# Optimization experiments

Measured on AMD Instinct MI355X. Metric: run time of the kernel, lower is better.

The kernel has to match this reference:

```python
import jax, jax.numpy as jnp
import numpy as np

# HeteNet distribute_compute reference: per-agent expert id (hete_pick) selects one of
# E heterogeneous expert MLPs; tokens are gathered per expert, run through that expert's
# actor net, and scattered back into a padded [n_threads, n_agents, n_action] output.
# Here each expert is a 2-layer MLP (Net._act actor head approximation):
#   logits = relu(x @ W1[e] + b1[e]) @ W2[e] + b2[e]
# The dispatch/combine is expressed as dense per-expert compute + one-hot combine,
# which is the mathematically identical (mask-select) form of the gather/scatter.

T, N, D, H, A, E = 64, 64, 512, 512, 32, 15  # threads, agents, obs_dim(+addon), hidden, actions, experts


def setup_inputs() -> dict:
    key = jax.random.key(0)
    k0, k1, k2, k3 = jax.random.split(key, 4)
    obs = jax.random.normal(k0, (T, N, D), dtype=jnp.float32)
    hete_pick = jax.random.randint(k1, (T, N), 0, E)  # expert id per agent
    W1 = jax.random.normal(k2, (E, D, H), dtype=jnp.float32) * (1.0 / np.sqrt(D))
    b1 = jnp.zeros((E, H), dtype=jnp.float32)
    W2 = jax.random.normal(k3, (E, H, A), dtype=jnp.float32) * (1.0 / np.sqrt(H))
    b2 = jnp.zeros((E, A), dtype=jnp.float32)
    return {"obs": obs, "W1": W1, "b1": b1, "W2": W2, "b2": b2, "hete_pick": hete_pick}


def reference(obs, W1, b1, W2, b2, hete_pick):
    # per-expert dense forward: [E, T, N, H]
    h = jax.nn.relu(jnp.einsum('tnd,edh->etnh', obs, W1) + b1[:, None, None, :])
    logits = jnp.einsum('etnh,eha->etna', h, W2) + b2[:, None, None, :]  # [E,T,N,A]
    # combine: scatter each expert's rows back per mask (hete_pick == e)
    onehot = (hete_pick[None, :, :] == jnp.arange(E)[:, None, None]).astype(obs.dtype)  # [E,T,N]
    return jnp.einsum('etna,etn->tna', logits, onehot)  # [T,N,A]
```

## Files before the change

### kernel.cpp

```cpp
#include <hip/hip_runtime.h>
#include <stdint.h>

#define NTOK 4096
#define DDIM 512
#define HDIM 512
#define ADIM 32
#define NEXP 15
#define TILE_M 32
#define GRID_M 288

typedef __attribute__((ext_vector_type(8))) short bf16x8;
typedef __attribute__((ext_vector_type(8))) unsigned short ushort8;
typedef __attribute__((ext_vector_type(4))) unsigned short ushort4v;
typedef __attribute__((ext_vector_type(4))) float f32x4;

__device__ __forceinline__ unsigned short f2bf(float f) {
  unsigned int u = __float_as_uint(f);
  u += 0x7fffu + ((u >> 16) & 1u);
  return (unsigned short)(u >> 16);
}

__device__ __forceinline__ void gld_lds16(const void* g, void* l) {
  __builtin_amdgcn_global_load_lds(
      (const __attribute__((address_space(1))) void*)g,
      (__attribute__((address_space(3))) void*)l, 16, 0, 0);
}

__global__ __launch_bounds__(256) void prep_kernel(
    const float* __restrict__ W1, const float* __restrict__ W2,
    const int* __restrict__ pick, int* __restrict__ meta,
    int* __restrict__ lists, unsigned short* __restrict__ W1I,
    unsigned short* __restrict__ W2T, float* __restrict__ out)
{
  extern __shared__ char smem[];
  const int bid = blockIdx.x;
  const int tid = threadIdx.x;
  const int x = bid & 7, s = bid >> 3;
  int role, e = 0, kc = 0;
  if (x < 7)       { role = 0; e = 2 * x + (s >> 4); kc = s & 15; }
  else if (s < 16) { role = 0; e = 14; kc = s; }
  else if (s < 31) { role = 1; e = s - 16; }
  else             { role = 2; }

  if (role == 0) {
    float* sm = (float*)smem;
    const int r0 = kc * 32;
    const float* src = W1 + (size_t)e * (DDIM * HDIM) + (size_t)r0 * HDIM;
    #pragma unroll
    for (int v = 0; v < 16; ++v) {
      int i = v * 256 + tid;
      int row = i >> 7, col = (i & 127) * 4;
      *(float4*)(sm + row * 517 + col) = *(const float4*)(src + (size_t)row * 512 + col);
    }
    __syncthreads();
    unsigned short* dst = W1I + (size_t)(e * 16 + kc) * 512 * 32;
    const int p = tid & 3;
    #pragma unroll
    for (int w = 0; w < 8; ++w) {
      int n = w * 64 + (tid >> 2);
      int q = p ^ ((n >> 1) & 3);
      ushort8 vv;
      #pragma unroll
      for (int xx = 0; xx < 8; ++xx) vv[xx] = f2bf(sm[(q * 8 + xx) * 517 + n]);
      *(ushort8*)(dst + (size_t)n * 32 + p * 8) = vv;
    }
  } else if (role == 1) {
    float4 z4; z4.x = 0.f; z4.y = 0.f; z4.z = 0.f; z4.w = 0.f;
    for (int i = e * 256 + tid; i < NTOK * ADIM / 4; i += 15 * 256)
      ((float4*)out)[i] = z4;
    float* sm = (float*)smem;
    const float* src = W2 + (size_t)e * (HDIM * ADIM);
    #pragma unroll
    for (int v = 0; v < 16; ++v) {
      int i = v * 256 + tid;
      int row = i >> 3, col = (i & 7) * 4;
      *(float4*)(sm + row * 36 + col) = *(const float4*)(src + (size_t)row * 32 + col);
    }
    __syncthreads();
    unsigned short* dst = W2T + (size_t)e * (ADIM * HDIM);
    const int a = tid >> 3, k0 = (tid & 7) * 64;
    #pragma unroll
    for (int w = 0; w < 8; ++w) {
      ushort8 vv;
      #pragma unroll
      for (int xx = 0; xx < 8; ++xx) vv[xx] = f2bf(sm[(size_t)(k0 + w * 8 + xx) * 36 + a]);
      *(ushort8*)(dst + (size_t)a * 512 + k0 + w * 8) = vv;
    }
  } else {
    int* s_pos = (int*)smem;
    int* s_wt  = s_pos + NEXP * 256;
    int* s_nt  = s_wt + 64;
    int* s_bse = s_nt + 16;
    const int lane = tid & 63, wv = tid >> 6;
    int pk[16];
    #pragma unroll
    for (int i = 0; i < 16; ++i) pk[i] = pick[tid * 16 + i];
    int c[NEXP], inc[NEXP];
    #pragma unroll
    for (int ee = 0; ee < NEXP; ++ee) {
      int cc = 0;
      #pragma unroll
      for (int i = 0; i < 16; ++i) cc += (pk[i] == ee) ? 1 : 0;
      c[ee] = cc; inc[ee] = cc;
    }
    #pragma unroll
    for (int off = 1; off < 64; off <<= 1) {
      #pragma unroll
      for (int ee = 0; ee < NEXP; ++ee) {
        int v = __shfl_up(inc[ee], off, 64);
        if (lane >= off) inc[ee] += v;
      }
    }
    if (lane == 63) {
      #pragma unroll
      for (int ee = 0; ee < NEXP; ++ee) s_wt[wv * 16 + ee] = inc[ee];
    }
    __syncthreads();
    #pragma unroll
    for (int ee = 0; ee < NEXP; ++ee) {
      int base0 = 0;
      #pragma unroll
      for (int w = 0; w < 4; ++w) if (w < wv) base0 += s_wt[w * 16 + ee];
      s_pos[ee * 256 + tid] = base0 + inc[ee] - c[ee];
    }
    #pragma unroll
    for (int i = 0; i < 16; ++i) {
      int pp = pk[i];
      int pos = s_pos[pp * 256 + tid]++;
      lists[pp * NTOK + pos] = tid * 16 + i;
    }
    if (tid < NEXP) {
      int tot = s_wt[tid] + s_wt[16 + tid] + s_wt[32 + tid] + s_wt[48 + tid];
      meta[tid] = tot;
      s_nt[tid] = (tot + TILE_M - 1) / TILE_M;
    }
    __syncthreads();
    if (tid == 0) {
      int b = 0;
      for (int ee = 0; ee < NEXP; ++ee) { s_bse[ee] = b; b += s_nt[ee]; }
      meta[15] = b;
    }
    __syncthreads();
    if (tid < NEXP) {
      int b = s_bse[tid], nt2 = s_nt[tid];
      for (int i = 0; i < nt2; ++i) meta[16 + b + i] = (tid << 16) | i;
    }
  }
}

__global__ __launch_bounds__(256, 2) void moe_gemm(
    const float* __restrict__ obs, const float* __restrict__ b1,
    const float* __restrict__ b2, const int* __restrict__ meta,
    const int* __restrict__ lists, const unsigned short* __restrict__ W1I,
    const unsigned short* __restrict__ W2T, float* __restrict__ out)
{
  const int ntiles = meta[15];
  const int nphys = ntiles * 2;
  const int p = blockIdx.x;
  const int xq = nphys >> 3, xr = nphys & 7;
  const int xcd = p & 7, slot = p >> 3;
  const int cx = xq + (xcd < xr ? 1 : 0);
  if (slot >= cx) return;
  const int j2 = xcd * xq + (xcd < xr ? xcd : xr) + slot;
  const int jt = j2 >> 1, half = j2 & 1;

  const int tl = meta[16 + jt];
  const int e = tl >> 16;
  const int tile_lo = (tl & 0xffff) * TILE_M;
  const int cnt = meta[e];
  int mvalid = cnt - tile_lo; if (mvalid > TILE_M) mvalid = TILE_M;

  extern __shared__ char smem[];
  char* s_x = smem;
  char* wb0 = smem + 32768;
  char* wb1 = smem + 49152;
  char* wb2 = smem + 65536;

  const int tid = threadIdx.x, lane = tid & 63, wave = tid >> 6;
  const int l15 = lane & 15, l4 = lane >> 4;
  const int nbl = wave * 64;
  const int hbase = half * 256;
  const int* mylist = lists + e * NTOK;
  const unsigned short* w1i_e = W1I + (size_t)e * 16 * 512 * 32;
  const unsigned short* w2t_e = W2T + (size_t)e * (ADIM * HDIM);

  const int m = tid >> 3, s8 = tid & 7;
  int idx = tile_lo + m; if (idx >= cnt) idx = cnt - 1;
  const float* grow = obs + (size_t)mylist[idx] * DDIM;
  float4 xf[16];
  #pragma unroll
  for (int si = 0; si < 8; ++si) {
    xf[si * 2]     = *(const float4*)(grow + (s8 + si * 8) * 8);
    xf[si * 2 + 1] = *(const float4*)(grow + (s8 + si * 8) * 8 + 4);
  }
  __builtin_amdgcn_sched_barrier(0);

  float4 bvv[4];
  #pragma unroll
  for (int nt = 0; nt < 4; ++nt)
    bvv[nt] = *(const float4*)(b1 + e * HDIM + hbase + nbl + nt * 16 + l4 * 4);
  __builtin_amdgcn_sched_barrier(0);

  auto issue_w1 = [&](int t, char* buf) {
    const unsigned short* wbase = w1i_e + (size_t)t * (512 * 32) + (size_t)hbase * 32;
    #pragma unroll
    for (int i = 0; i < 4; ++i) {
      int nb = nbl + i * 16;
      gld_lds16(wbase + (size_t)nb * 32 + lane * 8, buf + nb * 64);
    }
  };
  issue_w1(0, wb0);
  __builtin_amdgcn_sched_barrier(0);
  issue_w1(1, wb1);
  __builtin_amdgcn_sched_barrier(0);

  #pragma unroll
  for (int si = 0; si < 8; ++si) {
    int s = s8 + si * 8;
    float4 f0 = xf[si * 2], f1 = xf[si * 2 + 1];
    ushort8 v;
    v[0] = f2bf(f0.x); v[1] = f2bf(f0.y); v[2] = f2bf(f0.z); v[3] = f2bf(f0.w);
    v[4] = f2bf(f1.x); v[5] = f2bf(f1.y); v[6] = f2bf(f1.z); v[7] = f2bf(f1.w);
    *(ushort8*)(s_x + m * 1024 + ((s ^ (m & 7)) << 4)) = v;
  }
  __syncthreads();

  f32x4 acc[4][2];
  #pragma unroll
  for (int nt = 0; nt < 4; ++nt) {
    f32x4 b4 = {bvv[nt].x, bvv[nt].y, bvv[nt].z, bvv[nt].w};
    acc[nt][0] = b4; acc[nt][1] = b4;
  }

  #pragma unroll
  for (int t = 0; t < 16; ++t) {
    if (t < 14) {
      char* nxt = ((t + 2) % 3 == 0) ? wb0 : ((t + 2) % 3 == 1) ? wb1 : wb2;
      issue_w1(t + 2, nxt);
    } else if (t == 14) {
      #pragma unroll
      for (int i = 0; i < 4; ++i) {
        int o = wave * 4096 + i * 1024 + lane * 16;
        int a = o >> 9;
        int p16 = (o >> 4) & 31;
        gld_lds16(w2t_e + (size_t)a * 512 + hbase + (size_t)((p16 ^ (a & 7)) * 8),
                  wb1 + o);
      }
    }
    if (t < 15) asm volatile("s_waitcnt vmcnt(8)" ::: "memory");
    else        asm volatile("s_waitcnt vmcnt(4)" ::: "memory");
    __builtin_amdgcn_sched_barrier(0);

    const char* cw = (t % 3 == 0) ? wb0 : (t % 3 == 1) ? wb1 : wb2;
    bf16x8 wfr[4], xfr[2];
    #pragma unroll
    for (int nt = 0; nt < 4; ++nt) {
      int n = nbl + nt * 16 + l15;
      wfr[nt] = *(const bf16x8*)(cw + n * 64 + ((l4 ^ ((n >> 1) & 3)) << 4));
    }
    #pragma unroll
    for (int mt = 0; mt < 2; ++mt) {
      int mm = mt * 16 + l15;
      xfr[mt] = *(const bf16x8*)(s_x + mm * 1024 + ((((t << 2) + l4) ^ (mm & 7)) << 4));
    }
    #pragma unroll
    for (int nt = 0; nt < 4; ++nt)
      #pragma unroll
      for (int mt = 0; mt < 2; ++mt)
        acc[nt][mt] = __builtin_amdgcn_mfma_f32_16x16x32_bf16(wfr[nt], xfr[mt], acc[nt][mt], 0, 0, 0);
  }

  __syncthreads();

  #pragma unroll
  for (int nt = 0; nt < 4; ++nt) {
    int n0 = nbl + nt * 16 + l4 * 4;
    int sg = n0 >> 3, hsel = (n0 >> 2) & 1;
    #pragma unroll
    for (int mt = 0; mt < 2; ++mt) {
      int mm = mt * 16 + l15;
      ushort4v hv;
      #pragma unroll
      for (int r = 0; r < 4; ++r) hv[r] = f2bf(fmaxf(acc[nt][mt][r], 0.f));
      *(ushort4v*)(s_x + mm * 1024 + ((sg ^ (mm & 7)) << 4) + hsel * 8) = hv;
    }
  }
  __syncthreads();

  const int mt2 = wave >> 1, at2 = wave & 1;
  const int a2 = at2 * 16 + l15;
  float b2v = half ? 0.f : b2[e * ADIM + a2];
  f32x4 acc2 = {b2v, b2v, b2v, b2v};
  #pragma unroll
  for (int ks = 0; ks < 8; ++ks) {
    int mm = mt2 * 16 + l15;
    bf16x8 af = *(const bf16x8*)(s_x + mm * 1024 + ((((ks << 2) + l4) ^ (mm & 7)) << 4));
    bf16x8 bf = *(const bf16x8*)(wb1 + a2 * 512 + ((((ks << 2) + l4) ^ (a2 & 7)) << 4));
    acc2 = __builtin_amdgcn_mfma_f32_16x16x32_bf16(af, bf, acc2, 0, 0, 0);
  }
  #pragma unroll
  for (int r = 0; r < 4; ++r) {
    int mrow = mt2 * 16 + l4 * 4 + r;
    if (mrow < mvalid)
      atomicAdd(&out[(size_t)mylist[tile_lo + mrow] * ADIM + a2], acc2[r]);
  }
}

__global__ __launch_bounds__(256) void naive_kernel(
    const float* __restrict__ obs, const float* __restrict__ W1,
    const float* __restrict__ b1, const float* __restrict__ W2,
    const float* __restrict__ b2, const int* __restrict__ pick,
    float* __restrict__ out)
{
  __shared__ float sx[DDIM];
  __shared__ float sh[HDIM];
  const int t = blockIdx.x, tid = threadIdx.x;
  const int e = pick[t];
  const float* x = obs + (size_t)t * DDIM;
  for (int i = tid; i < DDIM; i += 256) sx[i] = x[i];
  __syncthreads();
  const float* w1 = W1 + (size_t)e * DDIM * HDIM;
  for (int j = tid; j < HDIM; j += 256) {
    float a = b1[e * HDIM + j];
    for (int d = 0; d < DDIM; ++d) a = fmaf(sx[d], w1[(size_t)d * HDIM + j], a);
    sh[j] = a > 0.f ? a : 0.f;
  }
  __syncthreads();
  if (tid < ADIM) {
    const float* w2 = W2 + (size_t)e * HDIM * ADIM;
    float a = b2[e * ADIM + tid];
    for (int j = 0; j < HDIM; ++j) a = fmaf(sh[j], w2[(size_t)j * ADIM + tid], a);
    out[(size_t)t * ADIM + tid] = a;
  }
}

extern "C" void kernel_launch(void* const* d_in, const int* in_sizes, int n_in,
                              void* d_out, int out_size, void* d_ws, size_t ws_size,
                              hipStream_t stream)
{
  const float* obs = (const float*)d_in[0];
  const float* W1  = (const float*)d_in[1];
  const float* b1  = (const float*)d_in[2];
  const float* W2  = (const float*)d_in[3];
  const float* b2  = (const float*)d_in[4];
  const int* pick  = (const int*)d_in[5];
  float* out = (float*)d_out;
  (void)in_sizes; (void)n_in; (void)out_size;

  const size_t OFF_LISTS = 1024;
  const size_t OFF_W1I   = 262144;
  const size_t OFF_W2T   = OFF_W1I + (size_t)NEXP * HDIM * DDIM * 2;
  const size_t WS_NEEDED = OFF_W2T + (size_t)NEXP * ADIM * HDIM * 2;

  if (ws_size < WS_NEEDED) {
    naive_kernel<<<dim3(NTOK), dim3(256), 0, stream>>>(obs, W1, b1, W2, b2, pick, out);
    return;
  }

  char* ws = (char*)d_ws;
  int* meta   = (int*)ws;
  int* lists  = (int*)(ws + OFF_LISTS);
  unsigned short* W1I = (unsigned short*)(ws + OFF_W1I);
  unsigned short* W2T = (unsigned short*)(ws + OFF_W2T);

  prep_kernel<<<dim3(256), dim3(256), 73728, stream>>>(
      W1, W2, pick, meta, lists, W1I, W2T, out);
  moe_gemm<<<dim3(GRID_M), dim3(256), 81920, stream>>>(
      obs, b1, b2, meta, lists, W1I, W2T, out);
}
```

Measured before the change: 25.42 us.

## Double token tile to 64 rows with 5-stage weight pipeline

Raises the per-block token tile from 32 to 64 rows, so each W1 slice streamed into LDS is reused across twice as many tokens, and deepens the LDS weight ring from 3 to 5 buffers with 4 tiles in flight. The obs load is now converted in a loop after the weight prefetch is issued, and the second GEMM gives each wave 16 rows across both action tiles. Costs are a larger LDS footprint (144KB), occupancy dropping to one block per CU, fewer blocks, and more padding waste on partially filled expert tiles.

```diff
diff --git a/kernel.cpp b/kernel.cpp
--- a/kernel.cpp
+++ b/kernel.cpp
@@ -6,8 +6,8 @@
 #define HDIM 512
 #define ADIM 32
 #define NEXP 15
-#define TILE_M 32
-#define GRID_M 288
+#define TILE_M 64
+#define GRID_M 160
 
 typedef __attribute__((ext_vector_type(8))) short bf16x8;
 typedef __attribute__((ext_vector_type(8))) unsigned short ushort8;
@@ -148,7 +148,7 @@
   }
 }
 
-__global__ __launch_bounds__(256, 2) void moe_gemm(
+__global__ __launch_bounds__(256, 1) void moe_gemm(
     const float* __restrict__ obs, const float* __restrict__ b1,
     const float* __restrict__ b2, const int* __restrict__ meta,
     const int* __restrict__ lists, const unsigned short* __restrict__ W1I,
@@ -172,9 +172,8 @@
 
   extern __shared__ char smem[];
   char* s_x = smem;
-  char* wb0 = smem + 32768;
-  char* wb1 = smem + 49152;
-  char* wb2 = smem + 65536;
+  char* wb[5] = { smem + 65536, smem + 81920, smem + 98304,
+                  smem + 114688, smem + 131072 };
 
   const int tid = threadIdx.x, lane = tid & 63, wave = tid >> 6;
   const int l15 = lane & 15, l4 = lane >> 4;
@@ -184,23 +183,6 @@
   const unsigned short* w1i_e = W1I + (size_t)e * 16 * 512 * 32;
   const unsigned short* w2t_e = W2T + (size_t)e * (ADIM * HDIM);
 
-  const int m = tid >> 3, s8 = tid & 7;
-  int idx = tile_lo + m; if (idx >= cnt) idx = cnt - 1;
-  const float* grow = obs + (size_t)mylist[idx] * DDIM;
-  float4 xf[16];
-  #pragma unroll
-  for (int si = 0; si < 8; ++si) {
-    xf[si * 2]     = *(const float4*)(grow + (s8 + si * 8) * 8);
-    xf[si * 2 + 1] = *(const float4*)(grow + (s8 + si * 8) * 8 + 4);
-  }
-  __builtin_amdgcn_sched_barrier(0);
-
-  float4 bvv[4];
-  #pragma unroll
-  for (int nt = 0; nt < 4; ++nt)
-    bvv[nt] = *(const float4*)(b1 + e * HDIM + hbase + nbl + nt * 16 + l4 * 4);
-  __builtin_amdgcn_sched_barrier(0);
-
   auto issue_w1 = [&](int t, char* buf) {
     const unsigned short* wbase = w1i_e + (size_t)t * (512 * 32) + (size_t)hbase * 32;
     #pragma unroll
@@ -209,64 +191,82 @@
       gld_lds16(wbase + (size_t)nb * 32 + lane * 8, buf + nb * 64);
     }
   };
-  issue_w1(0, wb0);
-  __builtin_amdgcn_sched_barrier(0);
-  issue_w1(1, wb1);
-  __builtin_amdgcn_sched_barrier(0);
-
-  #pragma unroll
-  for (int si = 0; si < 8; ++si) {
-    int s = s8 + si * 8;
-    float4 f0 = xf[si * 2], f1 = xf[si * 2 + 1];
-    ushort8 v;
-    v[0] = f2bf(f0.x); v[1] = f2bf(f0.y); v[2] = f2bf(f0.z); v[3] = f2bf(f0.w);
-    v[4] = f2bf(f1.x); v[5] = f2bf(f1.y); v[6] = f2bf(f1.z); v[7] = f2bf(f1.w);
-    *(ushort8*)(s_x + m * 1024 + ((s ^ (m & 7)) << 4)) = v;
-  }
-  __syncthreads();
-
-  f32x4 acc[4][2];
+  issue_w1(0, wb[0]);
+  __builtin_amdgcn_sched_barrier(0);
+  issue_w1(1, wb[1]);
+  __builtin_amdgcn_sched_barrier(0);
+  issue_w1(2, wb[2]);
+  __builtin_amdgcn_sched_barrier(0);
+  issue_w1(3, wb[3]);
+  __builtin_amdgcn_sched_barrier(0);
+
+  float4 bvv[4];
+  #pragma unroll
+  for (int nt = 0; nt < 4; ++nt)
+    bvv[nt] = *(const float4*)(b1 + e * HDIM + hbase + nbl + nt * 16 + l4 * 4);
+  __builtin_amdgcn_sched_barrier(0);
+
+  {
+    const int m = tid >> 2, sq = tid & 3;
+    int idx = tile_lo + m; if (idx >= cnt) idx = cnt - 1;
+    const float* grow = obs + (size_t)mylist[idx] * DDIM;
+    #pragma unroll 4
+    for (int si = 0; si < 16; ++si) {
+      const int s = sq + si * 4;
+      float4 f0 = *(const float4*)(grow + s * 8);
+      float4 f1 = *(const float4*)(grow + s * 8 + 4);
+      ushort8 v;
+      v[0] = f2bf(f0.x); v[1] = f2bf(f0.y); v[2] = f2bf(f0.z); v[3] = f2bf(f0.w);
+      v[4] = f2bf(f1.x); v[5] = f2bf(f1.y); v[6] = f2bf(f1.z); v[7] = f2bf(f1.w);
+      *(ushort8*)(s_x + m * 1024 + ((s ^ (m & 7)) << 4)) = v;
+    }
+  }
+  __syncthreads();
+
+  f32x4 acc[4][4];
   #pragma unroll
   for (int nt = 0; nt < 4; ++nt) {
     f32x4 b4 = {bvv[nt].x, bvv[nt].y, bvv[nt].z, bvv[nt].w};
-    acc[nt][0] = b4; acc[nt][1] = b4;
+    #pragma unroll
+    for (int mt = 0; mt < 4; ++mt) acc[nt][mt] = b4;
   }
 
   #pragma unroll
   for (int t = 0; t < 16; ++t) {
-    if (t < 14) {
-      char* nxt = ((t + 2) % 3 == 0) ? wb0 : ((t + 2) % 3 == 1) ? wb1 : wb2;
-      issue_w1(t + 2, nxt);
-    } else if (t == 14) {
+    if (t <= 11) {
+      issue_w1(t + 4, wb[(t + 4) % 5]);
+    } else if (t == 12) {
       #pragma unroll
       for (int i = 0; i < 4; ++i) {
         int o = wave * 4096 + i * 1024 + lane * 16;
         int a = o >> 9;
         int p16 = (o >> 4) & 31;
         gld_lds16(w2t_e + (size_t)a * 512 + hbase + (size_t)((p16 ^ (a & 7)) * 8),
-                  wb1 + o);
+                  wb[1] + o);
       }
     }
-    if (t < 15) asm volatile("s_waitcnt vmcnt(8)" ::: "memory");
-    else        asm volatile("s_waitcnt vmcnt(4)" ::: "memory");
+    if (t <= 12)      asm volatile("s_waitcnt vmcnt(16)" ::: "memory");
+    else if (t == 13) asm volatile("s_waitcnt vmcnt(12)" ::: "memory");
+    else if (t == 14) asm volatile("s_waitcnt vmcnt(8)" ::: "memory");
+    else              asm volatile("s_waitcnt vmcnt(4)" ::: "memory");
     __builtin_amdgcn_sched_barrier(0);
 
-    const char* cw = (t % 3 == 0) ? wb0 : (t % 3 == 1) ? wb1 : wb2;
-    bf16x8 wfr[4], xfr[2];
+    const char* cw = wb[t % 5];
+    bf16x8 wfr[4], xfr[4];
     #pragma unroll
     for (int nt = 0; nt < 4; ++nt) {
       int n = nbl + nt * 16 + l15;
       wfr[nt] = *(const bf16x8*)(cw + n * 64 + ((l4 ^ ((n >> 1) & 3)) << 4));
     }
     #pragma unroll
-    for (int mt = 0; mt < 2; ++mt) {
+    for (int mt = 0; mt < 4; ++mt) {
       int mm = mt * 16 + l15;
       xfr[mt] = *(const bf16x8*)(s_x + mm * 1024 + ((((t << 2) + l4) ^ (mm & 7)) << 4));
     }
     #pragma unroll
     for (int nt = 0; nt < 4; ++nt)
       #pragma unroll
-      for (int mt = 0; mt < 2; ++mt)
+      for (int mt = 0; mt < 4; ++mt)
         acc[nt][mt] = __builtin_amdgcn_mfma_f32_16x16x32_bf16(wfr[nt], xfr[mt], acc[nt][mt], 0, 0, 0);
   }
 
@@ -277,7 +277,7 @@
     int n0 = nbl + nt * 16 + l4 * 4;
     int sg = n0 >> 3, hsel = (n0 >> 2) & 1;
     #pragma unroll
-    for (int mt = 0; mt < 2; ++mt) {
+    for (int mt = 0; mt < 4; ++mt) {
       int mm = mt * 16 + l15;
       ushort4v hv;
       #pragma unroll
@@ -287,23 +287,32 @@
   }
   __syncthreads();
 
-  const int mt2 = wave >> 1, at2 = wave & 1;
-  const int a2 = at2 * 16 + l15;
-  float b2v = half ? 0.f : b2[e * ADIM + a2];
-  f32x4 acc2 = {b2v, b2v, b2v, b2v};
+  const int mm2 = wave * 16 + l15;
+  f32x4 acc2[2];
+  #pragma unroll
+  for (int at = 0; at < 2; ++at) {
+    float b2v = half ? 0.f : b2[e * ADIM + at * 16 + l15];
+    f32x4 b4 = {b2v, b2v, b2v, b2v};
+    acc2[at] = b4;
+  }
   #pragma unroll
   for (int ks = 0; ks < 8; ++ks) {
-    int mm = mt2 * 16 + l15;
-    bf16x8 af = *(const bf16x8*)(s_x + mm * 1024 + ((((ks << 2) + l4) ^ (mm & 7)) << 4));
-    bf16x8 bf = *(const bf16x8*)(wb1 + a2 * 512 + ((((ks << 2) + l4) ^ (a2 & 7)) << 4));
-    acc2 = __builtin_amdgcn_mfma_f32_16x16x32_bf16(af, bf, acc2, 0, 0, 0);
-  }
-  #pragma unroll
-  for (int r = 0; r < 4; ++r) {
-    int mrow = mt2 * 16 + l4 * 4 + r;
-    if (mrow < mvalid)
-      atomicAdd(&out[(size_t)mylist[tile_lo + mrow] * ADIM + a2], acc2[r]);
-  }
+    bf16x8 af = *(const bf16x8*)(s_x + mm2 * 1024 + ((((ks << 2) + l4) ^ (mm2 & 7)) << 4));
+    #pragma unroll
+    for (int at = 0; at < 2; ++at) {
+      int a = at * 16 + l15;
+      bf16x8 bf = *(const bf16x8*)(wb[1] + a * 512 + ((((ks << 2) + l4) ^ (a & 7)) << 4));
+      acc2[at] = __builtin_amdgcn_mfma_f32_16x16x32_bf16(af, bf, acc2[at], 0, 0, 0);
+    }
+  }
+  #pragma unroll
+  for (int at = 0; at < 2; ++at)
+    #pragma unroll
+    for (int r = 0; r < 4; ++r) {
+      int mrow = wave * 16 + l4 * 4 + r;
+      if (mrow < mvalid)
+        atomicAdd(&out[(size_t)mylist[tile_lo + mrow] * ADIM + at * 16 + l15], acc2[at][r]);
+    }
 }
 
 __global__ __launch_bounds__(256) void naive_kernel(
@@ -365,6 +374,6 @@
 
   prep_kernel<<<dim3(256), dim3(256), 73728, stream>>>(
       W1, W2, pick, meta, lists, W1I, W2T, out);
-  moe_gemm<<<dim3(GRID_M), dim3(256), 81920, stream>>>(
+  moe_gemm<<<dim3(GRID_M), dim3(256), 147456, stream>>>(
       obs, b1, b2, meta, lists, W1I, W2T, out);
 }
```

Measured after the change: 26.22 us. 1.03x slower.

## Move token routing from prep kernel into each GEMM block

Applied to the files above, without the earlier changes.

The single prep block that counted per-expert tokens and built global routing lists and tile metadata is removed. Each GEMM block now reads all 4096 expert picks, computes per-expert counts and tile mapping with wave reductions, and builds its own 32-token list in shared memory. This takes the serial routing block off the critical path and drops the global meta/list round trip, but every GEMM block now repeats the pick read and extra barriers before its main work.

```diff
diff --git a/kernel.cpp b/kernel.cpp
--- a/kernel.cpp
+++ b/kernel.cpp
@@ -28,9 +28,8 @@
 
 __global__ __launch_bounds__(256) void prep_kernel(
     const float* __restrict__ W1, const float* __restrict__ W2,
-    const int* __restrict__ pick, int* __restrict__ meta,
-    int* __restrict__ lists, unsigned short* __restrict__ W1I,
-    unsigned short* __restrict__ W2T, float* __restrict__ out)
+    unsigned short* __restrict__ W1I, unsigned short* __restrict__ W2T,
+    float* __restrict__ out)
 {
   extern __shared__ char smem[];
   const int bid = blockIdx.x;
@@ -40,7 +39,7 @@
   if (x < 7)       { role = 0; e = 2 * x + (s >> 4); kc = s & 15; }
   else if (s < 16) { role = 0; e = 14; kc = s; }
   else if (s < 31) { role = 1; e = s - 16; }
-  else             { role = 2; }
+  else             { return; }
 
   if (role == 0) {
     float* sm = (float*)smem;
@@ -64,7 +63,7 @@
       for (int xx = 0; xx < 8; ++xx) vv[xx] = f2bf(sm[(q * 8 + xx) * 517 + n]);
       *(ushort8*)(dst + (size_t)n * 32 + p * 8) = vv;
     }
-  } else if (role == 1) {
+  } else {
     float4 z4; z4.x = 0.f; z4.y = 0.f; z4.z = 0.f; z4.w = 0.f;
     for (int i = e * 256 + tid; i < NTOK * ADIM / 4; i += 15 * 256)
       ((float4*)out)[i] = z4;
@@ -86,75 +85,53 @@
       for (int xx = 0; xx < 8; ++xx) vv[xx] = f2bf(sm[(size_t)(k0 + w * 8 + xx) * 36 + a]);
       *(ushort8*)(dst + (size_t)a * 512 + k0 + w * 8) = vv;
     }
-  } else {
-    int* s_pos = (int*)smem;
-    int* s_wt  = s_pos + NEXP * 256;
-    int* s_nt  = s_wt + 64;
-    int* s_bse = s_nt + 16;
-    const int lane = tid & 63, wv = tid >> 6;
-    int pk[16];
-    #pragma unroll
-    for (int i = 0; i < 16; ++i) pk[i] = pick[tid * 16 + i];
-    int c[NEXP], inc[NEXP];
-    #pragma unroll
-    for (int ee = 0; ee < NEXP; ++ee) {
-      int cc = 0;
-      #pragma unroll
-      for (int i = 0; i < 16; ++i) cc += (pk[i] == ee) ? 1 : 0;
-      c[ee] = cc; inc[ee] = cc;
-    }
-    #pragma unroll
-    for (int off = 1; off < 64; off <<= 1) {
-      #pragma unroll
-      for (int ee = 0; ee < NEXP; ++ee) {
-        int v = __shfl_up(inc[ee], off, 64);
-        if (lane >= off) inc[ee] += v;
-      }
-    }
-    if (lane == 63) {
-      #pragma unroll
-      for (int ee = 0; ee < NEXP; ++ee) s_wt[wv * 16 + ee] = inc[ee];
-    }
-    __syncthreads();
-    #pragma unroll
-    for (int ee = 0; ee < NEXP; ++ee) {
-      int base0 = 0;
-      #pragma unroll
-      for (int w = 0; w < 4; ++w) if (w < wv) base0 += s_wt[w * 16 + ee];
-      s_pos[ee * 256 + tid] = base0 + inc[ee] - c[ee];
-    }
-    #pragma unroll
-    for (int i = 0; i < 16; ++i) {
-      int pp = pk[i];
-      int pos = s_pos[pp * 256 + tid]++;
-      lists[pp * NTOK + pos] = tid * 16 + i;
-    }
-    if (tid < NEXP) {
-      int tot = s_wt[tid] + s_wt[16 + tid] + s_wt[32 + tid] + s_wt[48 + tid];
-      meta[tid] = tot;
-      s_nt[tid] = (tot + TILE_M - 1) / TILE_M;
-    }
-    __syncthreads();
-    if (tid == 0) {
-      int b = 0;
-      for (int ee = 0; ee < NEXP; ++ee) { s_bse[ee] = b; b += s_nt[ee]; }
-      meta[15] = b;
-    }
-    __syncthreads();
-    if (tid < NEXP) {
-      int b = s_bse[tid], nt2 = s_nt[tid];
-      for (int i = 0; i < nt2; ++i) meta[16 + b + i] = (tid << 16) | i;
-    }
   }
 }
 
 __global__ __launch_bounds__(256, 2) void moe_gemm(
     const float* __restrict__ obs, const float* __restrict__ b1,
-    const float* __restrict__ b2, const int* __restrict__ meta,
-    const int* __restrict__ lists, const unsigned short* __restrict__ W1I,
-    const unsigned short* __restrict__ W2T, float* __restrict__ out)
+    const float* __restrict__ b2, const int* __restrict__ pick,
+    const unsigned short* __restrict__ W1I, const unsigned short* __restrict__ W2T,
+    float* __restrict__ out)
 {
-  const int ntiles = meta[15];
+  extern __shared__ char smem[];
+  char* s_x = smem;
+  char* wb0 = smem + 32768;
+  char* wb1 = smem + 49152;
+  char* wb2 = smem + 65536;
+  int* s_wt   = (int*)wb2;
+  int* s_we   = (int*)(wb2 + 256);
+  int* s_list = (int*)(wb2 + 320);
+
+  const int tid = threadIdx.x, lane = tid & 63, wave = tid >> 6;
+  const int l15 = lane & 15, l4 = lane >> 4;
+
+  int pk[16];
+  {
+    const int4* pv = (const int4*)pick + tid * 4;
+    int4 q0 = pv[0], q1 = pv[1], q2 = pv[2], q3 = pv[3];
+    pk[0]=q0.x; pk[1]=q0.y; pk[2]=q0.z; pk[3]=q0.w;
+    pk[4]=q1.x; pk[5]=q1.y; pk[6]=q1.z; pk[7]=q1.w;
+    pk[8]=q2.x; pk[9]=q2.y; pk[10]=q2.z; pk[11]=q2.w;
+    pk[12]=q3.x; pk[13]=q3.y; pk[14]=q3.z; pk[15]=q3.w;
+  }
+  #pragma unroll
+  for (int ee = 0; ee < NEXP; ++ee) {
+    int v = 0;
+    #pragma unroll
+    for (int i = 0; i < 16; ++i) v += (pk[i] == ee) ? 1 : 0;
+    #pragma unroll
+    for (int off = 1; off < 64; off <<= 1) v += __shfl_xor(v, off, 64);
+    if (lane == 0) s_wt[wave * 16 + ee] = v;
+  }
+  __syncthreads();
+  int ntl[NEXP], ntiles = 0;
+  #pragma unroll
+  for (int ee = 0; ee < NEXP; ++ee) {
+    int ct = s_wt[ee] + s_wt[16 + ee] + s_wt[32 + ee] + s_wt[48 + ee];
+    ntl[ee] = (ct + TILE_M - 1) >> 5;
+    ntiles += ntl[ee];
+  }
   const int nphys = ntiles * 2;
   const int p = blockIdx.x;
   const int xq = nphys >> 3, xr = nphys & 7;
@@ -163,30 +140,61 @@
   if (slot >= cx) return;
   const int j2 = xcd * xq + (xcd < xr ? xcd : xr) + slot;
   const int jt = j2 >> 1, half = j2 & 1;
-
-  const int tl = meta[16 + jt];
-  const int e = tl >> 16;
-  const int tile_lo = (tl & 0xffff) * TILE_M;
-  const int cnt = meta[e];
-  int mvalid = cnt - tile_lo; if (mvalid > TILE_M) mvalid = TILE_M;
-
-  extern __shared__ char smem[];
-  char* s_x = smem;
-  char* wb0 = smem + 32768;
-  char* wb1 = smem + 49152;
-  char* wb2 = smem + 65536;
-
-  const int tid = threadIdx.x, lane = tid & 63, wave = tid >> 6;
-  const int l15 = lane & 15, l4 = lane >> 4;
+  int e = 0, til = 0, cnte = 0, cum = 0, found = 0;
+  #pragma unroll
+  for (int ee = 0; ee < NEXP; ++ee) {
+    if (!found && jt < cum + ntl[ee]) {
+      e = ee; til = jt - cum;
+      cnte = s_wt[ee] + s_wt[16 + ee] + s_wt[32 + ee] + s_wt[48 + ee];
+      found = 1;
+    }
+    cum += ntl[ee];
+  }
+  const int tile_lo = til * TILE_M;
+  int mvalid = cnte - tile_lo; if (mvalid > TILE_M) mvalid = TILE_M;
+
+  {
+    int ce = 0;
+    #pragma unroll
+    for (int i = 0; i < 16; ++i) ce += (pk[i] == e) ? 1 : 0;
+    int inc = ce;
+    #pragma unroll
+    for (int off = 1; off < 64; off <<= 1) {
+      int v = __shfl_up(inc, off, 64);
+      if (lane >= off) inc += v;
+    }
+    if (lane == 63) s_we[wave] = inc;
+    __syncthreads();
+    int base0 = 0;
+    #pragma unroll
+    for (int w = 0; w < 4; ++w) if (w < wave) base0 += s_we[w];
+    int pos = base0 + inc - ce;
+    #pragma unroll
+    for (int i = 0; i < 16; ++i) {
+      if (pk[i] == e) {
+        int rel = pos - tile_lo;
+        if (rel >= 0 && rel < TILE_M) s_list[rel] = tid * 16 + i;
+        pos++;
+      }
+    }
+  }
+  __syncthreads();
+
+  const int mt2 = wave >> 1, at2 = wave & 1;
+  int tk[4];
+  #pragma unroll
+  for (int r = 0; r < 4; ++r) {
+    int mrow = mt2 * 16 + l4 * 4 + r;
+    tk[r] = s_list[mrow < mvalid ? mrow : 0];
+  }
+
   const int nbl = wave * 64;
   const int hbase = half * 256;
-  const int* mylist = lists + e * NTOK;
   const unsigned short* w1i_e = W1I + (size_t)e * 16 * 512 * 32;
   const unsigned short* w2t_e = W2T + (size_t)e * (ADIM * HDIM);
 
   const int m = tid >> 3, s8 = tid & 7;
-  int idx = tile_lo + m; if (idx >= cnt) idx = cnt - 1;
-  const float* grow = obs + (size_t)mylist[idx] * DDIM;
+  const float* grow = obs + (size_t)s_list[m < mvalid ? m : mvalid - 1] * DDIM;
   float4 xf[16];
   #pragma unroll
   for (int si = 0; si < 8; ++si) {
@@ -287,7 +295,6 @@
   }
   __syncthreads();
 
-  const int mt2 = wave >> 1, at2 = wave & 1;
   const int a2 = at2 * 16 + l15;
   float b2v = half ? 0.f : b2[e * ADIM + a2];
   f32x4 acc2 = {b2v, b2v, b2v, b2v};
@@ -302,7 +309,7 @@
   for (int r = 0; r < 4; ++r) {
     int mrow = mt2 * 16 + l4 * 4 + r;
     if (mrow < mvalid)
-      atomicAdd(&out[(size_t)mylist[tile_lo + mrow] * ADIM + a2], acc2[r]);
+      atomicAdd(&out[(size_t)tk[r] * ADIM + a2], acc2[r]);
   }
 }
 
@@ -347,7 +354,6 @@
   float* out = (float*)d_out;
   (void)in_sizes; (void)n_in; (void)out_size;
 
-  const size_t OFF_LISTS = 1024;
   const size_t OFF_W1I   = 262144;
   const size_t OFF_W2T   = OFF_W1I + (size_t)NEXP * HDIM * DDIM * 2;
   const size_t WS_NEEDED = OFF_W2T + (size_t)NEXP * ADIM * HDIM * 2;
@@ -358,13 +364,10 @@
   }
 
   char* ws = (char*)d_ws;
-  int* meta   = (int*)ws;
-  int* lists  = (int*)(ws + OFF_LISTS);
   unsigned short* W1I = (unsigned short*)(ws + OFF_W1I);
   unsigned short* W2T = (unsigned short*)(ws + OFF_W2T);
 
-  prep_kernel<<<dim3(256), dim3(256), 73728, stream>>>(
-      W1, W2, pick, meta, lists, W1I, W2T, out);
+  prep_kernel<<<dim3(256), dim3(256), 73728, stream>>>(W1, W2, W1I, W2T, out);
   moe_gemm<<<dim3(GRID_M), dim3(256), 81920, stream>>>(
-      obs, b1, b2, meta, lists, W1I, W2T, out);
-}
+      obs, b1, b2, pick, W1I, W2T, out);
+}
```

Result: slower. 30.50 us (+20.0%).
